# Optimization experiments

Measured on AMD Instinct MI355X. Metric: run time of the kernel, lower is better.

Reference implementation:

```python
import jax, jax.numpy as jnp
import numpy as np

FX, FY, CX, CY = 320.0, 320.0, 320.0, 240.0
N_MP, N_KF, M = 200000, 2000, 4000000


def setup_inputs() -> dict:
    key = jax.random.key(0)
    k1, k2, k3, k4 = jax.random.split(key, 4)
    # Map-point positions; shift to [1,2) so the homogeneous z after the (near-identity)
    # pose transform stays well away from zero for a stable perspective divide.
    tMP = jax.random.uniform(k1, (N_MP, 3), dtype=jnp.float32) + 1.0
    # Keyframe poses: identity + small perturbation (realistic SE3-like 4x4 matrices).
    tKF = jnp.eye(4, dtype=jnp.float32)[None] + 0.05 * jax.random.normal(k2, (N_KF, 4, 4), dtype=jnp.float32)
    # Measurement edges: (kf_id, mp_id) pairs.
    kf_ids = jax.random.randint(k3, (M,), 0, N_KF, dtype=jnp.int32)
    mp_ids = jax.random.randint(k4, (M,), 0, N_MP, dtype=jnp.int32)
    # Unique, sorted id columns (MPs[:,0] / KFs[:,0] in the original module).
    idxKF = jnp.arange(N_KF, dtype=jnp.int32)
    idxMP = jnp.arange(N_MP, dtype=jnp.int32)
    return {"tMP": tMP, "tKF": tKF, "kf_ids": kf_ids, "mp_ids": mp_ids,
            "idxKF": idxKF, "idxMP": idxMP}


def reference(tMP, tKF, kf_ids, mp_ids, idxKF, idxMP):
    # ID match. Original builds an O(M*N) boolean equality tensor and takes
    # torch.where(...)[1]; for unique sorted id arrays this is exactly a
    # sorted-index lookup, so we use searchsorted (same result, no huge temp).
    indexKF = jnp.searchsorted(idxKF, kf_ids)   # [M]
    indexMP = jnp.searchsorted(idxMP, mp_ids)   # [M]
    # Homogeneous map points: pad with 1 (F.pad(..., value=1) in original).
    tMPhomo = jnp.concatenate([tMP, jnp.ones((tMP.shape[0], 1), tMP.dtype)], axis=1)  # [N_MP,4]
    # Gather per-edge pose / point and do batched 4x4 @ 4 matvec.
    P = jnp.einsum('mij,mj->mi', tKF[indexKF], tMPhomo[indexMP])  # [M,4]
    # Perspective divide + intrinsics.
    ptx = P[:, 0] / P[:, 2] * FX + CX
    pty = P[:, 1] / P[:, 2] * FY + CY
    return jnp.stack([ptx, pty], axis=1)  # [M,2]
```

## Files before the change

### kernel.cpp

```cpp
#include <hip/hip_runtime.h>


#define FX_ 320.0f
#define FY_ 320.0f
#define CX_ 320.0f
#define CY_ 240.0f

#define MAX_KF 2000
#define MAIN_BLOCK 1024

__global__ __launch_bounds__(256) void mp_pack_kernel(
    const float* __restrict__ tMP, float4* __restrict__ tMPh, int N)
{
    int i = blockIdx.x * blockDim.x + threadIdx.x;
    if (i < N) {
        const float* p = tMP + (size_t)i * 3;
        tMPh[i] = make_float4(p[0], p[1], p[2], 1.0f);
    }
}

__global__ __launch_bounds__(MAIN_BLOCK) void ba_project_lds_kernel(
    const float4* __restrict__ tMPh,
    const float*  __restrict__ tKF,
    const int*    __restrict__ kf_ids,
    const int*    __restrict__ mp_ids,
    float* __restrict__ out,
    int M, int N_KF)
{
    __shared__ float4 sKF[MAX_KF * 3];

    int nChunks = N_KF * 3;
    for (int i = threadIdx.x; i < nChunks; i += MAIN_BLOCK) {
        int k = i / 3;
        int r = i - k * 3;
        sKF[i] = *reinterpret_cast<const float4*>(tKF + (size_t)k * 16 + r * 4);
    }
    __syncthreads();

    int t = blockIdx.x * MAIN_BLOCK + threadIdx.x;
    int m0 = t * 4;
    if (m0 + 3 < M) {
        int4 kf4 = *reinterpret_cast<const int4*>(kf_ids + m0);
        int4 mp4 = *reinterpret_cast<const int4*>(mp_ids + m0);
        int kf[4] = {kf4.x, kf4.y, kf4.z, kf4.w};
        int mp[4] = {mp4.x, mp4.y, mp4.z, mp4.w};
        float4 p[4];
        #pragma unroll
        for (int i = 0; i < 4; ++i) p[i] = tMPh[mp[i]];
        float res[8];
        #pragma unroll
        for (int i = 0; i < 4; ++i) {
            float4 r0 = sKF[kf[i] * 3 + 0];
            float4 r1 = sKF[kf[i] * 3 + 1];
            float4 r2 = sKF[kf[i] * 3 + 2];
            float P0 = fmaf(r0.x, p[i].x, fmaf(r0.y, p[i].y, fmaf(r0.z, p[i].z, r0.w)));
            float P1 = fmaf(r1.x, p[i].x, fmaf(r1.y, p[i].y, fmaf(r1.z, p[i].z, r1.w)));
            float P2 = fmaf(r2.x, p[i].x, fmaf(r2.y, p[i].y, fmaf(r2.z, p[i].z, r2.w)));
            float inv = 1.0f / P2;
            res[2 * i + 0] = fmaf(P0 * inv, FX_, CX_);
            res[2 * i + 1] = fmaf(P1 * inv, FY_, CY_);
        }
        float4* o = reinterpret_cast<float4*>(out + (size_t)m0 * 2);
        o[0] = make_float4(res[0], res[1], res[2], res[3]);
        o[1] = make_float4(res[4], res[5], res[6], res[7]);
    } else {
        for (int m = m0; m < M; ++m) {
            int kf = kf_ids[m];
            float4 p = tMPh[mp_ids[m]];
            float4 r0 = sKF[kf * 3 + 0];
            float4 r1 = sKF[kf * 3 + 1];
            float4 r2 = sKF[kf * 3 + 2];
            float P0 = fmaf(r0.x, p.x, fmaf(r0.y, p.y, fmaf(r0.z, p.z, r0.w)));
            float P1 = fmaf(r1.x, p.x, fmaf(r1.y, p.y, fmaf(r1.z, p.z, r1.w)));
            float P2 = fmaf(r2.x, p.x, fmaf(r2.y, p.y, fmaf(r2.z, p.z, r2.w)));
            float inv = 1.0f / P2;
            out[2 * (size_t)m + 0] = fmaf(P0 * inv, FX_, CX_);
            out[2 * (size_t)m + 1] = fmaf(P1 * inv, FY_, CY_);
        }
    }
}

__global__ __launch_bounds__(256) void ba_project_direct_kernel(
    const float* __restrict__ tMP, const float* __restrict__ tKF,
    const int* __restrict__ kf_ids, const int* __restrict__ mp_ids,
    float* __restrict__ out, int M)
{
    int t = blockIdx.x * blockDim.x + threadIdx.x;
    int m0 = t * 4;
    int mEnd = (m0 + 4 < M) ? (m0 + 4) : M;
    for (int m = m0; m < mEnd; ++m) {
        int kf = kf_ids[m];
        int mp = mp_ids[m];
        const float* K = tKF + (size_t)kf * 16;
        float4 r0 = *reinterpret_cast<const float4*>(K + 0);
        float4 r1 = *reinterpret_cast<const float4*>(K + 4);
        float4 r2 = *reinterpret_cast<const float4*>(K + 8);
        const float* p = tMP + (size_t)mp * 3;
        float x = p[0], y = p[1], z = p[2];
        float P0 = fmaf(r0.x, x, fmaf(r0.y, y, fmaf(r0.z, z, r0.w)));
        float P1 = fmaf(r1.x, x, fmaf(r1.y, y, fmaf(r1.z, z, r1.w)));
        float P2 = fmaf(r2.x, x, fmaf(r2.y, y, fmaf(r2.z, z, r2.w)));
        float inv = 1.0f / P2;
        out[2 * (size_t)m + 0] = fmaf(P0 * inv, FX_, CX_);
        out[2 * (size_t)m + 1] = fmaf(P1 * inv, FY_, CY_);
    }
}

extern "C" void kernel_launch(void* const* d_in, const int* in_sizes, int n_in,
                              void* d_out, int out_size, void* d_ws, size_t ws_size,
                              hipStream_t stream) {
    const float* tMP    = (const float*)d_in[0];
    const float* tKF    = (const float*)d_in[1];
    const int*   kf_ids = (const int*)d_in[2];
    const int*   mp_ids = (const int*)d_in[3];
    float* out = (float*)d_out;
    int M    = in_sizes[2];
    int N_MP = in_sizes[0] / 3;
    int N_KF = in_sizes[1] / 16;

    size_t need_ws = (size_t)N_MP * sizeof(float4);
    if (N_KF <= MAX_KF && ws_size >= need_ws) {
        float4* tMPh = (float4*)d_ws;
        mp_pack_kernel<<<(N_MP + 255) / 256, 256, 0, stream>>>(tMP, tMPh, N_MP);
        int threads = (M + 3) / 4;
        int grid = (threads + MAIN_BLOCK - 1) / MAIN_BLOCK;
        ba_project_lds_kernel<<<grid, MAIN_BLOCK, 0, stream>>>(
            tMPh, tKF, kf_ids, mp_ids, out, M, N_KF);
    } else {
        int threads = (M + 3) / 4;
        int grid = (threads + 255) / 256;
        ba_project_direct_kernel<<<grid, 256, 0, stream>>>(
            tMP, tKF, kf_ids, mp_ids, out, M);
    }
}
```

Before: 123.9 us.

## Use persistent grid-stride kernel to amortize LDS keyframe staging

Replaces the one-shot grid of 977 blocks, each reloading all keyframe poses into LDS, with a fixed 256-block persistent grid that loops over edges. Each thread now handles 8 edges per iteration instead of 4, giving more independent gathers in flight. The aim is to cut the repeated 96KB LDS fill per block. In exchange, 256 blocks of 1024 threads with 96KB LDS each may underfill the 256 CUs, since LDS limits each CU to one block, and the longer per-thread loop may expose gather latency.

```diff
diff --git a/kernel.cpp b/kernel.cpp
--- a/kernel.cpp
+++ b/kernel.cpp
@@ -8,6 +8,8 @@
 
 #define MAX_KF 2000
 #define MAIN_BLOCK 1024
+#define PERSIST_GRID 256
+#define EPT 8
 
 __global__ __launch_bounds__(256) void mp_pack_kernel(
     const float* __restrict__ tMP, float4* __restrict__ tMPh, int N)
@@ -19,7 +21,21 @@
     }
 }
 
-__global__ __launch_bounds__(MAIN_BLOCK) void ba_project_lds_kernel(
+__device__ __forceinline__ void project2(
+    const float4* sKF, int kf, const float4& p, float* rx, float* ry)
+{
+    float4 r0 = sKF[kf * 3 + 0];
+    float4 r1 = sKF[kf * 3 + 1];
+    float4 r2 = sKF[kf * 3 + 2];
+    float P0 = fmaf(r0.x, p.x, fmaf(r0.y, p.y, fmaf(r0.z, p.z, r0.w)));
+    float P1 = fmaf(r1.x, p.x, fmaf(r1.y, p.y, fmaf(r1.z, p.z, r1.w)));
+    float P2 = fmaf(r2.x, p.x, fmaf(r2.y, p.y, fmaf(r2.z, p.z, r2.w)));
+    float inv = 1.0f / P2;
+    *rx = fmaf(P0 * inv, FX_, CX_);
+    *ry = fmaf(P1 * inv, FY_, CY_);
+}
+
+__global__ __launch_bounds__(MAIN_BLOCK, 4) void ba_project_persist_kernel(
     const float4* __restrict__ tMPh,
     const float*  __restrict__ tKF,
     const int*    __restrict__ kf_ids,
@@ -37,45 +53,36 @@
     }
     __syncthreads();
 
-    int t = blockIdx.x * MAIN_BLOCK + threadIdx.x;
-    int m0 = t * 4;
-    if (m0 + 3 < M) {
-        int4 kf4 = *reinterpret_cast<const int4*>(kf_ids + m0);
-        int4 mp4 = *reinterpret_cast<const int4*>(mp_ids + m0);
-        int kf[4] = {kf4.x, kf4.y, kf4.z, kf4.w};
-        int mp[4] = {mp4.x, mp4.y, mp4.z, mp4.w};
-        float4 p[4];
-        #pragma unroll
-        for (int i = 0; i < 4; ++i) p[i] = tMPh[mp[i]];
-        float res[8];
-        #pragma unroll
-        for (int i = 0; i < 4; ++i) {
-            float4 r0 = sKF[kf[i] * 3 + 0];
-            float4 r1 = sKF[kf[i] * 3 + 1];
-            float4 r2 = sKF[kf[i] * 3 + 2];
-            float P0 = fmaf(r0.x, p[i].x, fmaf(r0.y, p[i].y, fmaf(r0.z, p[i].z, r0.w)));
-            float P1 = fmaf(r1.x, p[i].x, fmaf(r1.y, p[i].y, fmaf(r1.z, p[i].z, r1.w)));
-            float P2 = fmaf(r2.x, p[i].x, fmaf(r2.y, p[i].y, fmaf(r2.z, p[i].z, r2.w)));
-            float inv = 1.0f / P2;
-            res[2 * i + 0] = fmaf(P0 * inv, FX_, CX_);
-            res[2 * i + 1] = fmaf(P1 * inv, FY_, CY_);
-        }
-        float4* o = reinterpret_cast<float4*>(out + (size_t)m0 * 2);
-        o[0] = make_float4(res[0], res[1], res[2], res[3]);
-        o[1] = make_float4(res[4], res[5], res[6], res[7]);
-    } else {
-        for (int m = m0; m < M; ++m) {
-            int kf = kf_ids[m];
-            float4 p = tMPh[mp_ids[m]];
-            float4 r0 = sKF[kf * 3 + 0];
-            float4 r1 = sKF[kf * 3 + 1];
-            float4 r2 = sKF[kf * 3 + 2];
-            float P0 = fmaf(r0.x, p.x, fmaf(r0.y, p.y, fmaf(r0.z, p.z, r0.w)));
-            float P1 = fmaf(r1.x, p.x, fmaf(r1.y, p.y, fmaf(r1.z, p.z, r1.w)));
-            float P2 = fmaf(r2.x, p.x, fmaf(r2.y, p.y, fmaf(r2.z, p.z, r2.w)));
-            float inv = 1.0f / P2;
-            out[2 * (size_t)m + 0] = fmaf(P0 * inv, FX_, CX_);
-            out[2 * (size_t)m + 1] = fmaf(P1 * inv, FY_, CY_);
+    size_t tid = (size_t)blockIdx.x * MAIN_BLOCK + threadIdx.x;
+    size_t stride = (size_t)PERSIST_GRID * MAIN_BLOCK * EPT;
+
+    for (size_t m0 = tid * EPT; m0 < (size_t)M; m0 += stride) {
+        if (m0 + EPT <= (size_t)M) {
+            int4 kfa = *reinterpret_cast<const int4*>(kf_ids + m0);
+            int4 kfb = *reinterpret_cast<const int4*>(kf_ids + m0 + 4);
+            int4 mpa = *reinterpret_cast<const int4*>(mp_ids + m0);
+            int4 mpb = *reinterpret_cast<const int4*>(mp_ids + m0 + 4);
+            int kf[EPT] = {kfa.x, kfa.y, kfa.z, kfa.w, kfb.x, kfb.y, kfb.z, kfb.w};
+            int mp[EPT] = {mpa.x, mpa.y, mpa.z, mpa.w, mpb.x, mpb.y, mpb.z, mpb.w};
+            float4 p[EPT];
+            #pragma unroll
+            for (int i = 0; i < EPT; ++i) p[i] = tMPh[mp[i]];
+            float4* o = reinterpret_cast<float4*>(out + m0 * 2);
+            #pragma unroll
+            for (int i = 0; i < EPT; i += 2) {
+                float x0, y0, x1, y1;
+                project2(sKF, kf[i + 0], p[i + 0], &x0, &y0);
+                project2(sKF, kf[i + 1], p[i + 1], &x1, &y1);
+                o[i >> 1] = make_float4(x0, y0, x1, y1);
+            }
+        } else {
+            for (size_t m = m0; m < (size_t)M; ++m) {
+                float4 p = tMPh[mp_ids[m]];
+                float rx, ry;
+                project2(sKF, kf_ids[m], p, &rx, &ry);
+                out[m * 2 + 0] = rx;
+                out[m * 2 + 1] = ry;
+            }
         }
     }
 }
@@ -122,9 +129,7 @@
     if (N_KF <= MAX_KF && ws_size >= need_ws) {
         float4* tMPh = (float4*)d_ws;
         mp_pack_kernel<<<(N_MP + 255) / 256, 256, 0, stream>>>(tMP, tMPh, N_MP);
-        int threads = (M + 3) / 4;
-        int grid = (threads + MAIN_BLOCK - 1) / MAIN_BLOCK;
-        ba_project_lds_kernel<<<grid, MAIN_BLOCK, 0, stream>>>(
+        ba_project_persist_kernel<<<PERSIST_GRID, MAIN_BLOCK, 0, stream>>>(
             tMPh, tKF, kf_ids, mp_ids, out, M, N_KF);
     } else {
         int threads = (M + 3) / 4;
```

Result: faster. 121.5 us (-2.0%).
